# Optimization experiments

Hardware: AMD Instinct MI355X
Metric: run time of the kernel (lower is better)

Reference implementation:

```python
import jax, jax.numpy as jnp
import numpy as np
import math

B, S, HID = 2, 2048, 2048
NH, NKV, HD = 32, 8, 64
THETA = 10000.0
EPS = 1e-6
LAYER_IDX = 1
LAMBDA_INIT = 0.8 - 0.6 * math.exp(-0.3 * LAYER_IDX)
LAMBDA_STD = 0.1


def setup_inputs() -> dict:
    key = jax.random.key(0)
    ks = jax.random.split(key, 10)
    hidden_states = jax.random.normal(ks[0], (B, S, HID), jnp.float32)
    # RoPE cos/sin, llama convention: emb = cat(freqs, freqs)
    inv_freq = 1.0 / (THETA ** (np.arange(0, HD, 2, dtype=np.float32) / HD))
    freqs = np.outer(np.arange(S, dtype=np.float32), inv_freq)  # [S, HD/2]
    emb = np.concatenate([freqs, freqs], axis=-1)                # [S, HD]
    cos = jnp.broadcast_to(jnp.asarray(np.cos(emb), jnp.float32)[None], (B, S, HD))
    sin = jnp.broadcast_to(jnp.asarray(np.sin(emb), jnp.float32)[None], (B, S, HD))
    # additive causal mask [B,1,S,S]
    causal = jnp.triu(jnp.full((S, S), -1e9, dtype=jnp.float32), k=1)
    attention_mask = jnp.broadcast_to(causal[None, None], (B, 1, S, S))
    sc = 0.02
    wq = sc * jax.random.normal(ks[1], (NH * HD, HID), jnp.float32)
    wk = sc * jax.random.normal(ks[2], (NKV * HD, HID), jnp.float32)
    wv = sc * jax.random.normal(ks[3], (NKV * HD, HID), jnp.float32)
    wo = sc * jax.random.normal(ks[4], (HID, NH * HD), jnp.float32)
    lambda_q1 = LAMBDA_STD * jax.random.normal(ks[5], (HD,), jnp.float32)
    lambda_k1 = LAMBDA_STD * jax.random.normal(ks[6], (HD,), jnp.float32)
    lambda_q2 = LAMBDA_STD * jax.random.normal(ks[7], (HD,), jnp.float32)
    lambda_k2 = LAMBDA_STD * jax.random.normal(ks[8], (HD,), jnp.float32)
    return {"hidden_states": hidden_states, "cos": cos, "sin": sin,
            "attention_mask": attention_mask, "wq": wq, "wk": wk, "wv": wv,
            "wo": wo, "lambda_q1": lambda_q1, "lambda_k1": lambda_k1,
            "lambda_q2": lambda_q2, "lambda_k2": lambda_k2}


def _rotate_half(x):
    x1, x2 = jnp.split(x, 2, axis=-1)
    return jnp.concatenate([-x2, x1], axis=-1)


def reference(hidden_states, cos, sin, attention_mask, wq, wk, wv, wo,
              lambda_q1, lambda_k1, lambda_q2, lambda_k2):
    b, s, _ = hidden_states.shape
    # projections -> [b, h, s, d]
    q = jnp.einsum('bsh,oh->bso', hidden_states, wq).reshape(b, s, NH, HD).transpose(0, 2, 1, 3)
    k = jnp.einsum('bsh,oh->bso', hidden_states, wk).reshape(b, s, NKV, HD).transpose(0, 2, 1, 3)
    v = jnp.einsum('bsh,oh->bso', hidden_states, wv).reshape(b, s, NKV, HD).transpose(0, 2, 1, 3)
    # rotary
    c, sn = cos[:, None], sin[:, None]  # [b,1,s,d]
    q = q * c + _rotate_half(q) * sn
    k = k * c + _rotate_half(k) * sn
    # GQA repeat
    groups = NH // NKV
    k = jnp.repeat(k, groups, axis=1)
    v = jnp.repeat(v, groups, axis=1)
    # diff-attention value trick: pair head i with head i+NH/2 -> [b, NH, s, 2d]
    v = jnp.concatenate([v[:, :NH // 2], v[:, NH // 2:]], axis=-1)  # [b, NH/2, s, 2d]
    v = jnp.concatenate([v, v], axis=1)                              # [b, NH, s, 2d]
    # scores + causal mask, stable softmax in fp32
    aw = jnp.einsum('bhqd,bhkd->bhqk', q, k) / math.sqrt(HD)
    aw = aw + attention_mask
    aw = jax.nn.softmax(aw.astype(jnp.float32), axis=-1).astype(q.dtype)
    ao = jnp.einsum('bhqk,bhkd->bhqd', aw, v)  # [b, NH, s, 2d]
    lam1 = jnp.exp(jnp.sum((lambda_q1 * lambda_k1).astype(jnp.float32)))
    lam2 = jnp.exp(jnp.sum((lambda_q2 * lambda_k2).astype(jnp.float32)))
    lam = (lam1 - lam2).astype(q.dtype) + LAMBDA_INIT
    a1, a2 = ao[:, :NH // 2], ao[:, NH // 2:]
    out = a1 - lam * a2  # [b, NH/2, s, 2d]
    # RMSNorm over last dim (no affine)
    out = out * jax.lax.rsqrt(jnp.mean(out * out, axis=-1, keepdims=True) + EPS)
    out = (1.0 - LAMBDA_INIT) * out
    out = out.transpose(0, 2, 1, 3).reshape(b, s, NH * HD)
    return jnp.einsum('bso,ho->bsh', out, wo)
```

## Files before the change

### kernel.cpp

```cpp
#include <hip/hip_runtime.h>

typedef __attribute__((ext_vector_type(8))) short bhalf8;
typedef __attribute__((ext_vector_type(4))) float floatx4;

constexpr int B_ = 2, S_ = 2048, HID_ = 2048, NH_ = 32, NKV_ = 8, HD_ = 64;
constexpr float LAMBDA_INIT_F = 0.35550906759096924f;
constexpr float EPS_ = 1e-6f;
constexpr float QSCALE_ = 0.18033688011112042f;

#define DEVINL __device__ __forceinline__

DEVINL float bf2f(unsigned short u) {
    union { unsigned u; float f; } v; v.u = ((unsigned)u) << 16; return v.f;
}
DEVINL unsigned short f2bf(float f) {
    union { float f; unsigned u; } v; v.f = f;
    unsigned u = v.u;
    return (unsigned short)((u + 0x7fffu + ((u >> 16) & 1u)) >> 16);
}
DEVINL float fexp2(float x) {
#if __has_builtin(__builtin_amdgcn_exp2f)
    return __builtin_amdgcn_exp2f(x);
#else
    return exp2f(x);
#endif
}
DEVINL unsigned pk_bf16(float a, float b) {
#if __has_builtin(__builtin_amdgcn_cvt_pk_bf16_f32)
    typedef __bf16 bf16x2_t __attribute__((ext_vector_type(2)));
    bf16x2_t p = __builtin_amdgcn_cvt_pk_bf16_f32(a, b);
    unsigned r;
    __builtin_memcpy(&r, &p, 4);
    return r;
#else
    return (unsigned)f2bf(a) | ((unsigned)f2bf(b) << 16);
#endif
}
DEVINL void load_lds16(const unsigned short* g, unsigned short* l) {
    __builtin_amdgcn_global_load_lds(
        (const __attribute__((address_space(1))) unsigned int*)g,
        (__attribute__((address_space(3))) unsigned int*)l, 16, 0, 0);
}

__global__ __launch_bounds__(256)
void cvt_all(const float* __restrict__ hs, const float* __restrict__ wq,
             const float* __restrict__ wk, const float* __restrict__ wv,
             const float* __restrict__ wo, unsigned short* __restrict__ hs_bf,
             unsigned short* __restrict__ wcat, unsigned short* __restrict__ wo_bf,
             const float* __restrict__ lq1, const float* __restrict__ lk1,
             const float* __restrict__ lq2, const float* __restrict__ lk2,
             float* __restrict__ lam) {
    if (blockIdx.x == 18432) {
        const int l = threadIdx.x;
        if (l < 64) {
            float p1 = lq1[l] * lk1[l];
            float p2 = lq2[l] * lk2[l];
            #pragma unroll
            for (int off = 1; off < 64; off <<= 1) {
                p1 += __shfl_xor(p1, off, 64);
                p2 += __shfl_xor(p2, off, 64);
            }
            if (l == 0) *lam = expf(p1) - expf(p2) + LAMBDA_INIT_F;
        }
        return;
    }
    const size_t i = (size_t)(blockIdx.x * 256 + threadIdx.x) * 4;
    const float* src;
    unsigned short* dst;
    size_t off;
    float scale = 1.f;
    if (i < 8388608) { src = hs; dst = hs_bf; off = 0; }
    else if (i < 12582912) { src = wq; dst = wcat; off = 8388608; scale = QSCALE_; }
    else if (i < 13631488) { src = wk; dst = wcat + 4194304; off = 12582912; }
    else if (i < 14680064) { src = wv; dst = wcat + 5242880; off = 13631488; }
    else { src = wo; dst = wo_bf; off = 14680064; }
    const size_t k = i - off;
    const float4 v = *(const float4*)(src + k);
    ushort4 o;
    o.x = f2bf(v.x * scale); o.y = f2bf(v.y * scale);
    o.z = f2bf(v.z * scale); o.w = f2bf(v.w * scale);
    *(ushort4*)(dst + k) = o;
}

__global__ __launch_bounds__(256)
void gemm_qkv(const unsigned short* __restrict__ A, const unsigned short* __restrict__ Bw,
              const float* __restrict__ cosb, const float* __restrict__ sinb,
              unsigned short* __restrict__ Qr, unsigned short* __restrict__ Kr,
              unsigned short* __restrict__ VT) {
    constexpr int K = 2048;
    union GS {
        struct { unsigned short A[3][128][32]; unsigned short B[3][128][32]; } d;
        unsigned short vt[128][130];
    };
    __shared__ __align__(16) GS gsm;
    const int t = threadIdx.x;
    const int w = t >> 6, lane = t & 63, quad = lane >> 4, lid = lane & 15;
    const int wr = (w >> 1) * 64, wc = (w & 1) * 64;
    const long bm = (long)blockIdx.x * 128, bn = (long)blockIdx.y * 128;

    floatx4 acc[4][4];
    #pragma unroll
    for (int i = 0; i < 4; i++)
        #pragma unroll
        for (int j = 0; j < 4; j++) acc[i][j] = (floatx4){0.f, 0.f, 0.f, 0.f};

    const int s0 = t, s1 = t + 256;
    const unsigned short* Ag0 = A + (bm + (s0 >> 2)) * (long)K + (((s0 & 3) ^ ((s0 >> 3) & 3)) * 8);
    const unsigned short* Ag1 = A + (bm + (s1 >> 2)) * (long)K + (((s1 & 3) ^ ((s1 >> 3) & 3)) * 8);
    const unsigned short* Bg0 = Bw + (bn + (s0 >> 2)) * (long)K + (((s0 & 3) ^ ((s0 >> 3) & 3)) * 8);
    const unsigned short* Bg1 = Bw + (bn + (s1 >> 2)) * (long)K + (((s1 & 3) ^ ((s1 >> 3) & 3)) * 8);
    const int l0 = s0 * 8, l1 = s1 * 8;
    const int csw = (quad ^ ((lid >> 1) & 3)) * 8;

    load_lds16(Ag0, &gsm.d.A[0][0][0] + l0);
    load_lds16(Ag1, &gsm.d.A[0][0][0] + l1);
    load_lds16(Bg0, &gsm.d.B[0][0][0] + l0);
    load_lds16(Bg1, &gsm.d.B[0][0][0] + l1);
    load_lds16(Ag0 + 32, &gsm.d.A[1][0][0] + l0);
    load_lds16(Ag1 + 32, &gsm.d.A[1][0][0] + l1);
    load_lds16(Bg0 + 32, &gsm.d.B[1][0][0] + l0);
    load_lds16(Bg1 + 32, &gsm.d.B[1][0][0] + l1);

    const int nk = K >> 5;
    for (int kt = 0; kt < nk; kt++) {
        const int cur = kt % 3;
        if (kt + 1 == nk) asm volatile("s_waitcnt vmcnt(0)" ::: "memory");
        else              asm volatile("s_waitcnt vmcnt(4)" ::: "memory");
        __builtin_amdgcn_s_barrier();
        __builtin_amdgcn_sched_barrier(0);
        if (kt + 2 < nk) {
            const int nxt = (kt + 2) % 3;
            const int off = (kt + 2) << 5;
            load_lds16(Ag0 + off, &gsm.d.A[nxt][0][0] + l0);
            load_lds16(Ag1 + off, &gsm.d.A[nxt][0][0] + l1);
            load_lds16(Bg0 + off, &gsm.d.B[nxt][0][0] + l0);
            load_lds16(Bg1 + off, &gsm.d.B[nxt][0][0] + l1);
        }
        bhalf8 af[4], bf[4];
        #pragma unroll
        for (int i = 0; i < 4; i++) af[i] = *(const bhalf8*)&gsm.d.A[cur][wr + i * 16 + lid][csw];
        #pragma unroll
        for (int j = 0; j < 4; j++) bf[j] = *(const bhalf8*)&gsm.d.B[cur][wc + j * 16 + lid][csw];
        #pragma unroll
        for (int i = 0; i < 4; i++)
            #pragma unroll
            for (int j = 0; j < 4; j++)
                acc[i][j] = __builtin_amdgcn_mfma_f32_16x16x32_bf16(af[i], bf[j], acc[i][j], 0, 0, 0);
    }
    __syncthreads();

    const int y = blockIdx.y;
    if (y < 20) {
        const bool isQ = (y < 16);
        #pragma unroll
        for (int i = 0; i < 4; i++) {
            #pragma unroll
            for (int r = 0; r < 4; r++) {
                const long row = bm + wr + i * 16 + quad * 4 + r;
                const int bb = (int)(row >> 11), s = (int)(row & 2047);
                const float* cp = cosb + (size_t)row * 64;
                const float* sp = sinb + (size_t)row * 64;
                #pragma unroll
                for (int jj = 0; jj < 4; jj++) {
                    const int col = (int)bn + wc + jj * 16 + lid;
                    const int d = col & 63;
                    const float x = acc[i][jj][r];
                    const float oth = acc[i][jj ^ 2][r];
                    const float rot = (jj < 2) ? -oth : oth;
                    const float yv = x * cp[d] + rot * sp[d];
                    if (isQ) {
                        const int h = col >> 6;
                        Qr[((size_t)(bb * NH_ + h) * S_ + s) * HD_ + d] = f2bf(yv);
                    } else {
                        const int h = (col - 2048) >> 6;
                        Kr[((size_t)(bb * NKV_ + h) * S_ + s) * HD_ + d] = f2bf(yv);
                    }
                }
            }
        }
    } else {
        #pragma unroll
        for (int i = 0; i < 4; i++)
            #pragma unroll
            for (int jj = 0; jj < 4; jj++)
                #pragma unroll
                for (int r = 0; r < 4; r++)
                    gsm.vt[wr + i * 16 + quad * 4 + r][wc + jj * 16 + lid] = f2bf(acc[i][jj][r]);
        __syncthreads();
        const int b0 = (int)(bm >> 11), sbase = (int)(bm & 2047);
        #pragma unroll 4
        for (int it = 0; it < 32; it++) {
            const int d = w + 4 * it;
            const int colg = (int)bn + d;
            const int h = (colg - 2560) >> 6;
            const int dl = colg & 63;
            const int sl = lane * 2;
            const unsigned v = (unsigned)gsm.vt[sl][d] | ((unsigned)gsm.vt[sl + 1][d] << 16);
            *(unsigned*)(VT + ((size_t)(b0 * NKV_ + h) * HD_ + dl) * S_ + sbase + sl) = v;
        }
    }
}

__global__ __launch_bounds__(256)
void gemm_bt(const unsigned short* __restrict__ A, const unsigned short* __restrict__ Bw,
             float* __restrict__ Cout, int M, int N, int K) {
    __shared__ __align__(16) unsigned short As[3][128][32];
    __shared__ __align__(16) unsigned short Bs[3][128][32];
    const int t = threadIdx.x;
    const int w = t >> 6, lane = t & 63, quad = lane >> 4, lid = lane & 15;
    const int wr = (w >> 1) * 64, wc = (w & 1) * 64;
    const long bm = (long)blockIdx.x * 128, bn = (long)blockIdx.y * 128;

    floatx4 acc[4][4];
    #pragma unroll
    for (int i = 0; i < 4; i++)
        #pragma unroll
        for (int j = 0; j < 4; j++) acc[i][j] = (floatx4){0.f, 0.f, 0.f, 0.f};

    const int s0 = t, s1 = t + 256;
    const unsigned short* Ag0 = A + (bm + (s0 >> 2)) * (long)K + (((s0 & 3) ^ ((s0 >> 3) & 3)) * 8);
    const unsigned short* Ag1 = A + (bm + (s1 >> 2)) * (long)K + (((s1 & 3) ^ ((s1 >> 3) & 3)) * 8);
    const unsigned short* Bg0 = Bw + (bn + (s0 >> 2)) * (long)K + (((s0 & 3) ^ ((s0 >> 3) & 3)) * 8);
    const unsigned short* Bg1 = Bw + (bn + (s1 >> 2)) * (long)K + (((s1 & 3) ^ ((s1 >> 3) & 3)) * 8);
    const int l0 = s0 * 8, l1 = s1 * 8;
    const int csw = (quad ^ ((lid >> 1) & 3)) * 8;

    load_lds16(Ag0, &As[0][0][0] + l0);
    load_lds16(Ag1, &As[0][0][0] + l1);
    load_lds16(Bg0, &Bs[0][0][0] + l0);
    load_lds16(Bg1, &Bs[0][0][0] + l1);
    load_lds16(Ag0 + 32, &As[1][0][0] + l0);
    load_lds16(Ag1 + 32, &As[1][0][0] + l1);
    load_lds16(Bg0 + 32, &Bs[1][0][0] + l0);
    load_lds16(Bg1 + 32, &Bs[1][0][0] + l1);

    const int nk = K >> 5;
    for (int kt = 0; kt < nk; kt++) {
        const int cur = kt % 3;
        if (kt + 1 == nk) asm volatile("s_waitcnt vmcnt(0)" ::: "memory");
        else              asm volatile("s_waitcnt vmcnt(4)" ::: "memory");
        __builtin_amdgcn_s_barrier();
        __builtin_amdgcn_sched_barrier(0);
        if (kt + 2 < nk) {
            const int nxt = (kt + 2) % 3;
            const int off = (kt + 2) << 5;
            load_lds16(Ag0 + off, &As[nxt][0][0] + l0);
            load_lds16(Ag1 + off, &As[nxt][0][0] + l1);
            load_lds16(Bg0 + off, &Bs[nxt][0][0] + l0);
            load_lds16(Bg1 + off, &Bs[nxt][0][0] + l1);
        }
        bhalf8 af[4], bf[4];
        #pragma unroll
        for (int i = 0; i < 4; i++) af[i] = *(const bhalf8*)&As[cur][wr + i * 16 + lid][csw];
        #pragma unroll
        for (int j = 0; j < 4; j++) bf[j] = *(const bhalf8*)&Bs[cur][wc + j * 16 + lid][csw];
        #pragma unroll
        for (int i = 0; i < 4; i++)
            #pragma unroll
            for (int j = 0; j < 4; j++)
                acc[i][j] = __builtin_amdgcn_mfma_f32_16x16x32_bf16(af[i], bf[j], acc[i][j], 0, 0, 0);
    }

    #pragma unroll
    for (int i = 0; i < 4; i++) {
        #pragma unroll
        for (int j = 0; j < 4; j++) {
            const long row = bm + wr + i * 16 + quad * 4;
            const long col = bn + wc + j * 16 + lid;
            #pragma unroll
            for (int r = 0; r < 4; r++) Cout[(row + r) * N + col] = acc[i][j][r];
        }
    }
}

__global__ __launch_bounds__(512, 4)
void attn_diff(const unsigned short* __restrict__ Qr, const unsigned short* __restrict__ Kr,
               const unsigned short* __restrict__ VT, const float* __restrict__ lamp,
               unsigned short* __restrict__ attn) {
    union SM {
        struct {
            unsigned short Kt[2][64][72];
            unsigned short Vt[128][72];
            unsigned short Pt[8][16][72];
        } a;
        unsigned short Ot[2][64][132];
    };
    __shared__ __align__(16) SM sm;

    const int j = blockIdx.y, b = blockIdx.z;
    const int t = threadIdx.x;
    const int w = t >> 6, lane = t & 63, quad = lane >> 4, lid = lane & 15;
    const int st = w >> 2;
    const int rh = (w & 3) * 16;
    const int kv1 = j >> 2, kv2 = 4 + (j >> 2);
    const int qhead = j + st * 16;
    const float lam = *lamp;

    const int ss = t >> 8, kidx = t & 255;
    const int key_s = kidx >> 2, dh = (kidx & 3) * 16;
    const unsigned short* ksrc0 = Kr + (size_t)(b * NKV_ + (ss ? kv2 : kv1)) * S_ * HD_ +
                                  (size_t)key_s * HD_ + dh;
    const int d7 = t >> 2, vh = (t & 3) * 16;
    const unsigned short* vsrc0 = VT + ((size_t)(b * NKV_ + (d7 < 64 ? kv1 : kv2)) * HD_ +
                                        (d7 & 63)) * (size_t)S_ + vh;

    for (int half = 0; half < 2; half++) {
        const int qt = half ? (31 - (int)blockIdx.x) : (int)blockIdx.x;
        const int qb = qt * 64;

        const unsigned short* qbase =
            Qr + ((size_t)((b * NH_ + qhead) * S_) + qb + rh + lid) * HD_;
        const bhalf8 qa0 = *(const bhalf8*)(qbase + quad * 8);
        const bhalf8 qa1 = *(const bhalf8*)(qbase + 32 + quad * 8);

        floatx4 acc[8];
        #pragma unroll
        for (int c = 0; c < 8; c++) acc[c] = (floatx4){0.f, 0.f, 0.f, 0.f};
        float l_acc[4] = {0.f, 0.f, 0.f, 0.f};

        const int nkt = qt + 1;

        int4 kr0 = *(const int4*)(ksrc0);
        int4 kr1 = *(const int4*)(ksrc0 + 8);
        int4 vr0 = *(const int4*)(vsrc0);
        int4 vr1 = *(const int4*)(vsrc0 + 8);

        for (int kt = 0; kt < nkt; kt++) {
            asm volatile("s_waitcnt vmcnt(0)" ::: "memory");
            __builtin_amdgcn_s_barrier();
            __builtin_amdgcn_sched_barrier(0);
            *(int4*)&sm.a.Kt[ss][key_s][dh] = kr0;
            *(int4*)&sm.a.Kt[ss][key_s][dh + 8] = kr1;
            *(int4*)&sm.a.Vt[d7][vh] = vr0;
            *(int4*)&sm.a.Vt[d7][vh + 8] = vr1;
            if (kt + 1 < nkt) {
                const unsigned short* kp = ksrc0 + (size_t)(kt + 1) * 64 * HD_;
                const unsigned short* vp = vsrc0 + (kt + 1) * 64;
                kr0 = *(const int4*)(kp);
                kr1 = *(const int4*)(kp + 8);
                vr0 = *(const int4*)(vp);
                vr1 = *(const int4*)(vp + 8);
            }
            asm volatile("s_waitcnt lgkmcnt(0)" ::: "memory");
            __builtin_amdgcn_s_barrier();
            __builtin_amdgcn_sched_barrier(0);

            const bool last = (kt == nkt - 1);
            const int nt_lim = last ? ((w & 3) + 1) : 4;

            floatx4 sc[4];
            __builtin_amdgcn_s_setprio(1);
            #pragma unroll
            for (int nt = 0; nt < 4; nt++) {
                if (nt < nt_lim) {
                    const bhalf8 kb0 = *(const bhalf8*)&sm.a.Kt[st][nt * 16 + lid][quad * 8];
                    const bhalf8 kb1 = *(const bhalf8*)&sm.a.Kt[st][nt * 16 + lid][32 + quad * 8];
                    floatx4 z = (floatx4){0.f, 0.f, 0.f, 0.f};
                    z = __builtin_amdgcn_mfma_f32_16x16x32_bf16(qa0, kb0, z, 0, 0, 0);
                    z = __builtin_amdgcn_mfma_f32_16x16x32_bf16(qa1, kb1, z, 0, 0, 0);
                    sc[nt] = z;
                }
            }
            __builtin_amdgcn_s_setprio(0);

            if (last) {
                #pragma unroll
                for (int nt = 0; nt < 4; nt++) {
                    const int keyg = kt * 64 + nt * 16 + lid;
                    #pragma unroll
                    for (int r = 0; r < 4; r++) {
                        float p = 0.f;
                        if (nt < nt_lim) {
                            const int rowg = qb + rh + quad * 4 + r;
                            p = (keyg > rowg) ? 0.f : fexp2(sc[nt][r]);
                        }
                        sc[nt][r] = p;
                        l_acc[r] += p;
                    }
                }
            } else {
                #pragma unroll
                for (int nt = 0; nt < 4; nt++)
                    #pragma unroll
                    for (int r = 0; r < 4; r++) {
                        const float p = fexp2(sc[nt][r]);
                        sc[nt][r] = p;
                        l_acc[r] += p;
                    }
            }

            #pragma unroll
            for (int nt = 0; nt < 4; nt++) {
                #pragma unroll
                for (int r = 0; r < 4; r += 2) {
                    const unsigned pk = pk_bf16(sc[nt][r], sc[nt][r + 1]);
                    sm.a.Pt[w][quad * 4 + r][nt * 16 + lid] = (unsigned short)(pk & 0xffff);
                    sm.a.Pt[w][quad * 4 + r + 1][nt * 16 + lid] = (unsigned short)(pk >> 16);
                }
            }

            __builtin_amdgcn_s_setprio(1);
            #pragma unroll
            for (int kk = 0; kk < 2; kk++) {
                if (nt_lim > kk * 2) {
                    const bhalf8 pa = *(const bhalf8*)&sm.a.Pt[w][lid][kk * 32 + quad * 8];
                    #pragma unroll
                    for (int c = 0; c < 8; c++) {
                        const bhalf8 vb = *(const bhalf8*)&sm.a.Vt[c * 16 + lid][kk * 32 + quad * 8];
                        acc[c] = __builtin_amdgcn_mfma_f32_16x16x32_bf16(pa, vb, acc[c], 0, 0, 0);
                    }
                }
            }
            __builtin_amdgcn_s_setprio(0);
        }

        #pragma unroll
        for (int off = 1; off < 16; off <<= 1)
            #pragma unroll
            for (int r = 0; r < 4; r++) l_acc[r] += __shfl_xor(l_acc[r], off, 64);

        __syncthreads();
        #pragma unroll
        for (int r = 0; r < 4; r++) {
            const float rl = 1.0f / l_acc[r];
            #pragma unroll
            for (int c = 0; c < 8; c++)
                sm.Ot[st][rh + quad * 4 + r][c * 16 + lid] = f2bf(acc[c][r] * rl);
        }
        __syncthreads();

        const int row = t >> 3, m = t & 7;
        float vals[16];
        float ssum = 0.f;
        #pragma unroll
        for (int c = 0; c < 4; c++) {
            const unsigned long long u0 = *(const unsigned long long*)&sm.Ot[0][row][m * 4 + 32 * c];
            const unsigned long long u1 = *(const unsigned long long*)&sm.Ot[1][row][m * 4 + 32 * c];
            #pragma unroll
            for (int i = 0; i < 4; i++) {
                const float x = bf2f((unsigned short)(u0 >> (16 * i))) -
                                lam * bf2f((unsigned short)(u1 >> (16 * i)));
                vals[c * 4 + i] = x;
                ssum += x * x;
            }
        }
        ssum += __shfl_xor(ssum, 1, 64);
        ssum += __shfl_xor(ssum, 2, 64);
        ssum += __shfl_xor(ssum, 4, 64);
        const float scale = (1.f - LAMBDA_INIT_F) * rsqrtf(ssum * (1.f / 128.f) + EPS_);
        unsigned short* dst = attn + (size_t)(b * S_ + qb + row) * (NH_ * HD_) + j * 128 + m * 4;
        #pragma unroll
        for (int c = 0; c < 4; c++) {
            unsigned short ob[4];
            #pragma unroll
            for (int i = 0; i < 4; i++) ob[i] = f2bf(vals[c * 4 + i] * scale);
            *(unsigned long long*)(dst + 32 * c) = *(const unsigned long long*)ob;
        }
        __syncthreads();
    }
}

extern "C" void kernel_launch(void* const* d_in, const int* in_sizes, int n_in,
                              void* d_out, int out_size, void* d_ws, size_t ws_size,
                              hipStream_t stream) {
    const float* hs   = (const float*)d_in[0];
    const float* cosb = (const float*)d_in[1];
    const float* sinb = (const float*)d_in[2];
    const float* wq   = (const float*)d_in[4];
    const float* wk   = (const float*)d_in[5];
    const float* wv   = (const float*)d_in[6];
    const float* wo   = (const float*)d_in[7];
    const float* lq1  = (const float*)d_in[8];
    const float* lk1  = (const float*)d_in[9];
    const float* lq2  = (const float*)d_in[10];
    const float* lk2  = (const float*)d_in[11];

    unsigned short* p = (unsigned short*)d_ws;
    unsigned short* hs_bf = p;  p += (size_t)4096 * 2048;
    unsigned short* wcat  = p;  p += (size_t)3072 * 2048;
    unsigned short* wo_bf = p;  p += (size_t)2048 * 2048;
    unsigned short* Qr    = p;  p += (size_t)B_ * NH_ * S_ * HD_;
    unsigned short* Kr    = p;  p += (size_t)B_ * NKV_ * S_ * HD_;
    unsigned short* VT    = p;  p += (size_t)B_ * NKV_ * S_ * HD_;
    unsigned short* attnb = p;  p += (size_t)4096 * 2048;
    float* lam = (float*)p;

    cvt_all<<<18433, 256, 0, stream>>>(hs, wq, wk, wv, wo, hs_bf, wcat, wo_bf,
                                       lq1, lk1, lq2, lk2, lam);
    gemm_qkv<<<dim3(32, 24), 256, 0, stream>>>(hs_bf, wcat, cosb, sinb, Qr, Kr, VT);
    attn_diff<<<dim3(16, 16, 2), 512, 0, stream>>>(Qr, Kr, VT, lam, attnb);
    gemm_bt<<<dim3(32, 16), 256, 0, stream>>>(attnb, wo_bf, (float*)d_out, 4096, 2048, 2048);
}
```

Before: 347.6 us.

## Enlarge GEMM tiles to 256x256 with 512 threads and double-buffered K=64 stages

Both the QKV projection GEMM and the output projection GEMM switch to 256x256 block tiles with 8 waves, a 64-wide K step, double buffering, and an XOR-swizzled LDS layout. The inner loop splits into sub-steps with explicit lgkmcnt waits, setprio around the MFMAs, and barriers. The V-transpose epilogue is done in two passes through LDS to fit the larger tile. The aim is more data reuse per block and fewer global loads, at the cost of far fewer blocks than CUs and higher register pressure.

```diff
diff --git a/kernel.cpp b/kernel.cpp
--- a/kernel.cpp
+++ b/kernel.cpp
@@ -4,6 +4,7 @@
 typedef __attribute__((ext_vector_type(4))) float floatx4;
 
 constexpr int B_ = 2, S_ = 2048, HID_ = 2048, NH_ = 32, NKV_ = 8, HD_ = 64;
+constexpr int GK = 2048;
 constexpr float LAMBDA_INIT_F = 0.35550906759096924f;
 constexpr float EPS_ = 1e-6f;
 constexpr float QSCALE_ = 0.18033688011112042f;
@@ -82,91 +83,118 @@
     *(ushort4*)(dst + k) = o;
 }
 
-__global__ __launch_bounds__(256)
+
+__global__ __launch_bounds__(512, 2)
 void gemm_qkv(const unsigned short* __restrict__ A, const unsigned short* __restrict__ Bw,
               const float* __restrict__ cosb, const float* __restrict__ sinb,
               unsigned short* __restrict__ Qr, unsigned short* __restrict__ Kr,
               unsigned short* __restrict__ VT) {
-    constexpr int K = 2048;
     union GS {
-        struct { unsigned short A[3][128][32]; unsigned short B[3][128][32]; } d;
-        unsigned short vt[128][130];
+        struct { unsigned short A[2][16384]; unsigned short B[2][16384]; } d;
+        unsigned short vt[128][258];
     };
-    __shared__ __align__(16) GS gsm;
+    __shared__ __align__(16) GS g;
     const int t = threadIdx.x;
     const int w = t >> 6, lane = t & 63, quad = lane >> 4, lid = lane & 15;
-    const int wr = (w >> 1) * 64, wc = (w & 1) * 64;
-    const long bm = (long)blockIdx.x * 128, bn = (long)blockIdx.y * 128;
-
-    floatx4 acc[4][4];
-    #pragma unroll
-    for (int i = 0; i < 4; i++)
-        #pragma unroll
-        for (int j = 0; j < 4; j++) acc[i][j] = (floatx4){0.f, 0.f, 0.f, 0.f};
-
-    const int s0 = t, s1 = t + 256;
-    const unsigned short* Ag0 = A + (bm + (s0 >> 2)) * (long)K + (((s0 & 3) ^ ((s0 >> 3) & 3)) * 8);
-    const unsigned short* Ag1 = A + (bm + (s1 >> 2)) * (long)K + (((s1 & 3) ^ ((s1 >> 3) & 3)) * 8);
-    const unsigned short* Bg0 = Bw + (bn + (s0 >> 2)) * (long)K + (((s0 & 3) ^ ((s0 >> 3) & 3)) * 8);
-    const unsigned short* Bg1 = Bw + (bn + (s1 >> 2)) * (long)K + (((s1 & 3) ^ ((s1 >> 3) & 3)) * 8);
-    const int l0 = s0 * 8, l1 = s1 * 8;
-    const int csw = (quad ^ ((lid >> 1) & 3)) * 8;
-
-    load_lds16(Ag0, &gsm.d.A[0][0][0] + l0);
-    load_lds16(Ag1, &gsm.d.A[0][0][0] + l1);
-    load_lds16(Bg0, &gsm.d.B[0][0][0] + l0);
-    load_lds16(Bg1, &gsm.d.B[0][0][0] + l1);
-    load_lds16(Ag0 + 32, &gsm.d.A[1][0][0] + l0);
-    load_lds16(Ag1 + 32, &gsm.d.A[1][0][0] + l1);
-    load_lds16(Bg0 + 32, &gsm.d.B[1][0][0] + l0);
-    load_lds16(Bg1 + 32, &gsm.d.B[1][0][0] + l1);
-
-    const int nk = K >> 5;
+    const int wrr = (w >> 2) * 128;
+    const int wcn = (w & 3) * 64;
+    const long bm = (long)blockIdx.x * 256, bn = (long)blockIdx.y * 256;
+
+    int aoff[4], boff[4];
+    #pragma unroll
+    for (int i = 0; i < 4; i++) {
+        const int slot = i * 512 + t;
+        const int row = slot >> 3, p = slot & 7;
+        const int c = p ^ (row & 7);
+        aoff[i] = (int)((bm + row) * GK) + c * 8;
+        boff[i] = (int)((bn + row) * GK) + c * 8;
+    }
+    #pragma unroll
+    for (int i = 0; i < 4; i++) load_lds16(A + aoff[i], &g.d.A[0][0] + (i * 512 + t) * 8);
+    #pragma unroll
+    for (int i = 0; i < 4; i++) load_lds16(Bw + boff[i], &g.d.B[0][0] + (i * 512 + t) * 8);
+    #pragma unroll
+    for (int i = 0; i < 4; i++) load_lds16(A + aoff[i] + 64, &g.d.A[1][0] + (i * 512 + t) * 8);
+    #pragma unroll
+    for (int i = 0; i < 4; i++) load_lds16(Bw + boff[i] + 64, &g.d.B[1][0] + (i * 512 + t) * 8);
+
+    floatx4 acc[8][4];
+    #pragma unroll
+    for (int m = 0; m < 8; m++)
+        #pragma unroll
+        for (int n = 0; n < 4; n++) acc[m][n] = (floatx4){0.f, 0.f, 0.f, 0.f};
+
+    const int nk = GK >> 6;
     for (int kt = 0; kt < nk; kt++) {
-        const int cur = kt % 3;
-        if (kt + 1 == nk) asm volatile("s_waitcnt vmcnt(0)" ::: "memory");
-        else              asm volatile("s_waitcnt vmcnt(4)" ::: "memory");
+        const unsigned short* Ab = &g.d.A[kt & 1][0];
+        const unsigned short* Bb = &g.d.B[kt & 1][0];
+        if (kt + 1 < nk) asm volatile("s_waitcnt vmcnt(8)" ::: "memory");
+        else             asm volatile("s_waitcnt vmcnt(0)" ::: "memory");
         __builtin_amdgcn_s_barrier();
         __builtin_amdgcn_sched_barrier(0);
+
+        bhalf8 bf[4];
+        #pragma unroll
+        for (int ks = 0; ks < 2; ks++) {
+            #pragma unroll
+            for (int mh = 0; mh < 2; mh++) {
+                if (mh == 0) {
+                    #pragma unroll
+                    for (int n = 0; n < 4; n++) {
+                        const int row = wcn + n * 16 + lid;
+                        bf[n] = *(const bhalf8*)&Bb[row * 64 + ((ks * 4 + quad) ^ (lid & 7)) * 8];
+                    }
+                }
+                bhalf8 af[4];
+                #pragma unroll
+                for (int mi = 0; mi < 4; mi++) {
+                    const int row = wrr + (mh * 4 + mi) * 16 + lid;
+                    af[mi] = *(const bhalf8*)&Ab[row * 64 + ((ks * 4 + quad) ^ (lid & 7)) * 8];
+                }
+                asm volatile("s_waitcnt lgkmcnt(0)" ::: "memory");
+                __builtin_amdgcn_sched_barrier(0);
+                __builtin_amdgcn_s_setprio(1);
+                #pragma unroll
+                for (int mi = 0; mi < 4; mi++)
+                    #pragma unroll
+                    for (int n = 0; n < 4; n++)
+                        acc[mh * 4 + mi][n] =
+                            __builtin_amdgcn_mfma_f32_16x16x32_bf16(af[mi], bf[n], acc[mh * 4 + mi][n], 0, 0, 0);
+                __builtin_amdgcn_s_setprio(0);
+                __builtin_amdgcn_s_barrier();
+                __builtin_amdgcn_sched_barrier(0);
+            }
+        }
         if (kt + 2 < nk) {
-            const int nxt = (kt + 2) % 3;
-            const int off = (kt + 2) << 5;
-            load_lds16(Ag0 + off, &gsm.d.A[nxt][0][0] + l0);
-            load_lds16(Ag1 + off, &gsm.d.A[nxt][0][0] + l1);
-            load_lds16(Bg0 + off, &gsm.d.B[nxt][0][0] + l0);
-            load_lds16(Bg1 + off, &gsm.d.B[nxt][0][0] + l1);
-        }
-        bhalf8 af[4], bf[4];
-        #pragma unroll
-        for (int i = 0; i < 4; i++) af[i] = *(const bhalf8*)&gsm.d.A[cur][wr + i * 16 + lid][csw];
-        #pragma unroll
-        for (int j = 0; j < 4; j++) bf[j] = *(const bhalf8*)&gsm.d.B[cur][wc + j * 16 + lid][csw];
-        #pragma unroll
-        for (int i = 0; i < 4; i++)
-            #pragma unroll
-            for (int j = 0; j < 4; j++)
-                acc[i][j] = __builtin_amdgcn_mfma_f32_16x16x32_bf16(af[i], bf[j], acc[i][j], 0, 0, 0);
+            const int off = (kt + 2) * 64;
+            unsigned short* Ad = &g.d.A[kt & 1][0];
+            unsigned short* Bd = &g.d.B[kt & 1][0];
+            #pragma unroll
+            for (int i = 0; i < 4; i++) load_lds16(A + aoff[i] + off, Ad + (i * 512 + t) * 8);
+            #pragma unroll
+            for (int i = 0; i < 4; i++) load_lds16(Bw + boff[i] + off, Bd + (i * 512 + t) * 8);
+        }
     }
     __syncthreads();
 
     const int y = blockIdx.y;
-    if (y < 20) {
-        const bool isQ = (y < 16);
-        #pragma unroll
-        for (int i = 0; i < 4; i++) {
+    if (y < 10) {
+        const bool isQ = (y < 8);
+        #pragma unroll
+        for (int m = 0; m < 8; m++) {
             #pragma unroll
             for (int r = 0; r < 4; r++) {
-                const long row = bm + wr + i * 16 + quad * 4 + r;
+                const long row = bm + wrr + m * 16 + quad * 4 + r;
                 const int bb = (int)(row >> 11), s = (int)(row & 2047);
                 const float* cp = cosb + (size_t)row * 64;
                 const float* sp = sinb + (size_t)row * 64;
                 #pragma unroll
-                for (int jj = 0; jj < 4; jj++) {
-                    const int col = (int)bn + wc + jj * 16 + lid;
+                for (int n = 0; n < 4; n++) {
+                    const int col = (int)bn + wcn + n * 16 + lid;
                     const int d = col & 63;
-                    const float x = acc[i][jj][r];
-                    const float oth = acc[i][jj ^ 2][r];
-                    const float rot = (jj < 2) ? -oth : oth;
+                    const float x = acc[m][n][r];
+                    const float oth = acc[m][n ^ 2][r];
+                    const float rot = (n < 2) ? -oth : oth;
                     const float yv = x * cp[d] + rot * sp[d];
                     if (isQ) {
                         const int h = col >> 6;
@@ -179,96 +207,130 @@
             }
         }
     } else {
-        #pragma unroll
-        for (int i = 0; i < 4; i++)
-            #pragma unroll
-            for (int jj = 0; jj < 4; jj++)
-                #pragma unroll
-                for (int r = 0; r < 4; r++)
-                    gsm.vt[wr + i * 16 + quad * 4 + r][wc + jj * 16 + lid] = f2bf(acc[i][jj][r]);
-        __syncthreads();
-        const int b0 = (int)(bm >> 11), sbase = (int)(bm & 2047);
-        #pragma unroll 4
-        for (int it = 0; it < 32; it++) {
-            const int d = w + 4 * it;
-            const int colg = (int)bn + d;
-            const int h = (colg - 2560) >> 6;
-            const int dl = colg & 63;
-            const int sl = lane * 2;
-            const unsigned v = (unsigned)gsm.vt[sl][d] | ((unsigned)gsm.vt[sl + 1][d] << 16);
-            *(unsigned*)(VT + ((size_t)(b0 * NKV_ + h) * HD_ + dl) * S_ + sbase + sl) = v;
-        }
-    }
-}
-
-__global__ __launch_bounds__(256)
+        const int b0 = (int)(bm >> 11);
+        const int sb = (int)(bm & 2047);
+        #pragma unroll
+        for (int pass = 0; pass < 2; pass++) {
+            if ((w >> 2) == pass) {
+                #pragma unroll
+                for (int m = 0; m < 8; m++)
+                    #pragma unroll
+                    for (int n = 0; n < 4; n++)
+                        #pragma unroll
+                        for (int r = 0; r < 4; r++)
+                            g.vt[m * 16 + quad * 4 + r][wcn + n * 16 + lid] = f2bf(acc[m][n][r]);
+            }
+            __syncthreads();
+            #pragma unroll 4
+            for (int it = 0; it < 32; it++) {
+                const int d = w + 8 * it;
+                const int colg = (int)bn + d;
+                const int h = (colg - 2560) >> 6;
+                const int dl = colg & 63;
+                const int sl = lane * 2;
+                const unsigned v = (unsigned)g.vt[sl][d] | ((unsigned)g.vt[sl + 1][d] << 16);
+                *(unsigned*)(VT + ((size_t)(b0 * NKV_ + h) * HD_ + dl) * S_ + sb + pass * 128 + sl) = v;
+            }
+            __syncthreads();
+        }
+    }
+}
+
+__global__ __launch_bounds__(512, 2)
 void gemm_bt(const unsigned short* __restrict__ A, const unsigned short* __restrict__ Bw,
              float* __restrict__ Cout, int M, int N, int K) {
-    __shared__ __align__(16) unsigned short As[3][128][32];
-    __shared__ __align__(16) unsigned short Bs[3][128][32];
+    __shared__ __align__(16) unsigned short As[2][16384];
+    __shared__ __align__(16) unsigned short Bs[2][16384];
     const int t = threadIdx.x;
     const int w = t >> 6, lane = t & 63, quad = lane >> 4, lid = lane & 15;
-    const int wr = (w >> 1) * 64, wc = (w & 1) * 64;
-    const long bm = (long)blockIdx.x * 128, bn = (long)blockIdx.y * 128;
-
-    floatx4 acc[4][4];
-    #pragma unroll
-    for (int i = 0; i < 4; i++)
-        #pragma unroll
-        for (int j = 0; j < 4; j++) acc[i][j] = (floatx4){0.f, 0.f, 0.f, 0.f};
-
-    const int s0 = t, s1 = t + 256;
-    const unsigned short* Ag0 = A + (bm + (s0 >> 2)) * (long)K + (((s0 & 3) ^ ((s0 >> 3) & 3)) * 8);
-    const unsigned short* Ag1 = A + (bm + (s1 >> 2)) * (long)K + (((s1 & 3) ^ ((s1 >> 3) & 3)) * 8);
-    const unsigned short* Bg0 = Bw + (bn + (s0 >> 2)) * (long)K + (((s0 & 3) ^ ((s0 >> 3) & 3)) * 8);
-    const unsigned short* Bg1 = Bw + (bn + (s1 >> 2)) * (long)K + (((s1 & 3) ^ ((s1 >> 3) & 3)) * 8);
-    const int l0 = s0 * 8, l1 = s1 * 8;
-    const int csw = (quad ^ ((lid >> 1) & 3)) * 8;
-
-    load_lds16(Ag0, &As[0][0][0] + l0);
-    load_lds16(Ag1, &As[0][0][0] + l1);
-    load_lds16(Bg0, &Bs[0][0][0] + l0);
-    load_lds16(Bg1, &Bs[0][0][0] + l1);
-    load_lds16(Ag0 + 32, &As[1][0][0] + l0);
-    load_lds16(Ag1 + 32, &As[1][0][0] + l1);
-    load_lds16(Bg0 + 32, &Bs[1][0][0] + l0);
-    load_lds16(Bg1 + 32, &Bs[1][0][0] + l1);
-
-    const int nk = K >> 5;
+    const int wrr = (w >> 2) * 128;
+    const int wcn = (w & 3) * 64;
+    const long bm = (long)blockIdx.x * 256, bn = (long)blockIdx.y * 256;
+
+    int aoff[4], boff[4];
+    #pragma unroll
+    for (int i = 0; i < 4; i++) {
+        const int slot = i * 512 + t;
+        const int row = slot >> 3, p = slot & 7;
+        const int c = p ^ (row & 7);
+        aoff[i] = (int)((bm + row) * GK) + c * 8;
+        boff[i] = (int)((bn + row) * GK) + c * 8;
+    }
+    #pragma unroll
+    for (int i = 0; i < 4; i++) load_lds16(A + aoff[i], &As[0][0] + (i * 512 + t) * 8);
+    #pragma unroll
+    for (int i = 0; i < 4; i++) load_lds16(Bw + boff[i], &Bs[0][0] + (i * 512 + t) * 8);
+    #pragma unroll
+    for (int i = 0; i < 4; i++) load_lds16(A + aoff[i] + 64, &As[1][0] + (i * 512 + t) * 8);
+    #pragma unroll
+    for (int i = 0; i < 4; i++) load_lds16(Bw + boff[i] + 64, &Bs[1][0] + (i * 512 + t) * 8);
+
+    floatx4 acc[8][4];
+    #pragma unroll
+    for (int m = 0; m < 8; m++)
+        #pragma unroll
+        for (int n = 0; n < 4; n++) acc[m][n] = (floatx4){0.f, 0.f, 0.f, 0.f};
+
+    const int nk = GK >> 6;
     for (int kt = 0; kt < nk; kt++) {
-        const int cur = kt % 3;
-        if (kt + 1 == nk) asm volatile("s_waitcnt vmcnt(0)" ::: "memory");
-        else              asm volatile("s_waitcnt vmcnt(4)" ::: "memory");
+        const unsigned short* Ab = &As[kt & 1][0];
+        const unsigned short* Bb = &Bs[kt & 1][0];
+        if (kt + 1 < nk) asm volatile("s_waitcnt vmcnt(8)" ::: "memory");
+        else             asm volatile("s_waitcnt vmcnt(0)" ::: "memory");
         __builtin_amdgcn_s_barrier();
         __builtin_amdgcn_sched_barrier(0);
+
+        bhalf8 bf[4];
+        #pragma unroll
+        for (int ks = 0; ks < 2; ks++) {
+            #pragma unroll
+            for (int mh = 0; mh < 2; mh++) {
+                if (mh == 0) {
+                    #pragma unroll
+                    for (int n = 0; n < 4; n++) {
+                        const int row = wcn + n * 16 + lid;
+                        bf[n] = *(const bhalf8*)&Bb[row * 64 + ((ks * 4 + quad) ^ (lid & 7)) * 8];
+                    }
+                }
+                bhalf8 af[4];
+                #pragma unroll
+                for (int mi = 0; mi < 4; mi++) {
+                    const int row = wrr + (mh * 4 + mi) * 16 + lid;
+                    af[mi] = *(const bhalf8*)&Ab[row * 64 + ((ks * 4 + quad) ^ (lid & 7)) * 8];
+                }
+                asm volatile("s_waitcnt lgkmcnt(0)" ::: "memory");
+                __builtin_amdgcn_sched_barrier(0);
+                __builtin_amdgcn_s_setprio(1);
+                #pragma unroll
+                for (int mi = 0; mi < 4; mi++)
+                    #pragma unroll
+                    for (int n = 0; n < 4; n++)
+                        acc[mh * 4 + mi][n] =
+                            __builtin_amdgcn_mfma_f32_16x16x32_bf16(af[mi], bf[n], acc[mh * 4 + mi][n], 0, 0, 0);
+                __builtin_amdgcn_s_setprio(0);
+                __builtin_amdgcn_s_barrier();
+                __builtin_amdgcn_sched_barrier(0);
+            }
+        }
         if (kt + 2 < nk) {
-            const int nxt = (kt + 2) % 3;
-            const int off = (kt + 2) << 5;
-            load_lds16(Ag0 + off, &As[nxt][0][0] + l0);
-            load_lds16(Ag1 + off, &As[nxt][0][0] + l1);
-            load_lds16(Bg0 + off, &Bs[nxt][0][0] + l0);
-            load_lds16(Bg1 + off, &Bs[nxt][0][0] + l1);
-        }
-        bhalf8 af[4], bf[4];
-        #pragma unroll
-        for (int i = 0; i < 4; i++) af[i] = *(const bhalf8*)&As[cur][wr + i * 16 + lid][csw];
-        #pragma unroll
-        for (int j = 0; j < 4; j++) bf[j] = *(const bhalf8*)&Bs[cur][wc + j * 16 + lid][csw];
-        #pragma unroll
-        for (int i = 0; i < 4; i++)
-            #pragma unroll
-            for (int j = 0; j < 4; j++)
-                acc[i][j] = __builtin_amdgcn_mfma_f32_16x16x32_bf16(af[i], bf[j], acc[i][j], 0, 0, 0);
-    }
-
-    #pragma unroll
-    for (int i = 0; i < 4; i++) {
-        #pragma unroll
-        for (int j = 0; j < 4; j++) {
-            const long row = bm + wr + i * 16 + quad * 4;
-            const long col = bn + wc + j * 16 + lid;
-            #pragma unroll
-            for (int r = 0; r < 4; r++) Cout[(row + r) * N + col] = acc[i][j][r];
+            const int off = (kt + 2) * 64;
+            unsigned short* Ad = &As[kt & 1][0];
+            unsigned short* Bd = &Bs[kt & 1][0];
+            #pragma unroll
+            for (int i = 0; i < 4; i++) load_lds16(A + aoff[i] + off, Ad + (i * 512 + t) * 8);
+            #pragma unroll
+            for (int i = 0; i < 4; i++) load_lds16(Bw + boff[i] + off, Bd + (i * 512 + t) * 8);
+        }
+    }
+
+    #pragma unroll
+    for (int m = 0; m < 8; m++) {
+        #pragma unroll
+        for (int n = 0; n < 4; n++) {
+            const long row = bm + wrr + m * 16 + quad * 4;
+            const long col = bn + wcn + n * 16 + lid;
+            #pragma unroll
+            for (int r = 0; r < 4; r++) Cout[(row + r) * N + col] = acc[m][n][r];
         }
     }
 }
@@ -487,7 +549,7 @@
 
     cvt_all<<<18433, 256, 0, stream>>>(hs, wq, wk, wv, wo, hs_bf, wcat, wo_bf,
                                        lq1, lk1, lq2, lk2, lam);
-    gemm_qkv<<<dim3(32, 24), 256, 0, stream>>>(hs_bf, wcat, cosb, sinb, Qr, Kr, VT);
+    gemm_qkv<<<dim3(16, 12), 512, 0, stream>>>(hs_bf, wcat, cosb, sinb, Qr, Kr, VT);
     attn_diff<<<dim3(16, 16, 2), 512, 0, stream>>>(Qr, Kr, VT, lam, attnb);
-    gemm_bt<<<dim3(32, 16), 256, 0, stream>>>(attnb, wo_bf, (float*)d_out, 4096, 2048, 2048);
-}
+    gemm_bt<<<dim3(16, 8), 512, 0, stream>>>(attnb, wo_bf, (float*)d_out, 4096, 2048, 2048);
+}
```

Result: slower. 371.0 us (+6.7%).
